# Kernel tuning notes

Measured on AMD Instinct MI355X. Metric: run time of the kernel, lower is better.

The kernel has to match this reference:

```python
import jax, jax.numpy as jnp
import numpy as np

B, C, H, W = 8, 256, 128, 128
P = 7          # patch_size (odd)
N = 500        # n_infer (eval mode)
HIDDEN = C // 16  # reduction=16


def setup_inputs() -> dict:
    key = jax.random.key(0)
    ks = jax.random.split(key, 8)
    def s(k, shape, fan_in):
        return jax.random.normal(k, shape, jnp.float32) * (1.0 / np.sqrt(fan_in))
    return {
        "x_main": jax.random.normal(ks[0], (B, C, H, W), jnp.float32),
        "x_aux": jax.random.normal(ks[1], (B, C, H, W), jnp.float32),
        "scorer_w": s(ks[2], (C,), C),            # 1x1 conv C->1
        "scorer_b": s(ks[3], (1,), C),
        "fc1_w": s(ks[4], (3 * C, HIDDEN), 3 * C),
        "fc1_b": jnp.zeros((HIDDEN,), jnp.float32),
        "fc2_w": s(ks[5], (HIDDEN, C), HIDDEN),
        "fc2_b": jnp.zeros((C,), jnp.float32),
        "proj_w": s(ks[6], (C, C), C),
        "proj_b": jnp.zeros((C,), jnp.float32),
        "n": N,
    }


def _sample_patch_feats(feat, px, py):
    # feat: [C,H,W]; px,py: [n,p,p] pixel coords (align_corners=False convention).
    # Bilinear sample with zero padding, then pool 0.5*(mean+max) over the patch.
    c, h, w = feat.shape
    x0 = jnp.floor(px); y0 = jnp.floor(py)
    wx1 = px - x0; wy1 = py - y0
    def gather(yi, xi):
        valid = ((yi >= 0) & (yi < h) & (xi >= 0) & (xi < w)).astype(feat.dtype)
        yc = jnp.clip(yi, 0, h - 1).astype(jnp.int32)
        xc = jnp.clip(xi, 0, w - 1).astype(jnp.int32)
        return feat[:, yc, xc] * valid  # [C,n,p,p]
    patch = (gather(y0, x0) * ((1 - wy1) * (1 - wx1))
             + gather(y0, x0 + 1) * ((1 - wy1) * wx1)
             + gather(y0 + 1, x0) * (wy1 * (1 - wx1))
             + gather(y0 + 1, x0 + 1) * (wy1 * wx1))  # [C,n,p,p]
    v = 0.5 * (patch.mean(axis=(2, 3)) + patch.max(axis=(2, 3)))  # [C,n]
    return v.T  # [n,C]


def reference(x_main, x_aux, scorer_w, scorer_b, fc1_w, fc1_b, fc2_w, fc2_b, proj_w, proj_b, n):
    b, c, h, w = x_main.shape
    # saliency scores -> topk indices over flattened HW
    score = jax.nn.sigmoid(jnp.einsum('bchw,c->bhw', x_main, scorer_w) + scorer_b[0])
    score = score.reshape(b, h * w)
    _, idx = jax.lax.top_k(score, n)  # [b,n] int32
    idx_y = idx // w
    idx_x = idx - idx_y * w
    # build the (clamped) normalized grid exactly as the torch module does,
    # then convert to pixel coords: px = ((g+1)*W - 1)/2 (align_corners=False)
    r = P // 2
    d = jnp.arange(-r, r + 1, dtype=jnp.float32)
    yy, xx = jnp.meshgrid(d, d, indexing='ij')
    off_x = xx * (2.0 / w); off_y = yy * (2.0 / h)           # [p,p]
    cx = (idx_x.astype(jnp.float32) + 0.5) * (2.0 / w) - 1.0  # [b,n]
    cy = (idx_y.astype(jnp.float32) + 0.5) * (2.0 / h) - 1.0
    gx = jnp.clip(cx[:, :, None, None] + off_x, -1.0, 1.0)    # [b,n,p,p]
    gy = jnp.clip(cy[:, :, None, None] + off_y, -1.0, 1.0)
    px = ((gx + 1.0) * w - 1.0) * 0.5
    py = ((gy + 1.0) * h - 1.0) * 0.5
    sample = jax.vmap(_sample_patch_feats)
    v_main = sample(x_main, px, py)  # [b,n,C]
    v_aux = sample(x_aux, px, py)    # aux_in_proj is Identity (c_main==c_aux)
    # instance-level cross attention
    sim = jnp.einsum('bnc,bmc->bnm', v_main, v_aux) / jnp.sqrt(jnp.float32(c))
    attn = jax.nn.softmax(sim, axis=-1)
    v_hat = jnp.einsum('bnm,bmc->bnc', attn, v_aux)
    # gated fusion MLP
    z = jnp.concatenate([v_main, v_hat, v_main - v_hat], axis=-1)  # [b,n,3C]
    gate = jax.nn.sigmoid(jax.nn.relu(z @ fc1_w + fc1_b) @ fc2_w + fc2_b)
    v_fused = v_main + gate * (v_main - v_hat)
    v_inj = v_fused @ proj_w + proj_b  # [b,n,C]
    # scatter-add reinjection at the topk locations
    inject = jnp.zeros((b, h * w, c), x_main.dtype)
    inject = inject.at[jnp.arange(b)[:, None], idx].add(v_inj)
    inject = inject.reshape(b, h, w, c).transpose(0, 3, 1, 2)
    return x_main + inject
```

## Files before the change

kernel.cpp:

```cpp
#include <hip/hip_runtime.h>
#include <cstdint>
#include <cstddef>

#define HW    16384
#define CCH   256
#define WID   128
#define NB    8
#define NSEL  500
#define NPAD  512
#define CPG   16

__device__ __forceinline__ unsigned key_of(float f) {
  unsigned u = __float_as_uint(f);
  return (u & 0x80000000u) ? ~u : (u | 0x80000000u);
}

__global__ __launch_bounds__(256) void score_copy_kernel(const float* __restrict__ x,
                                                         const float* __restrict__ w,
                                                         float* __restrict__ logits,
                                                         float* __restrict__ out) {
  __shared__ float ws[CCH];
  int tid = threadIdx.x;
  ws[tid] = w[tid];
  __syncthreads();
  int pix = blockIdx.x * 256 + tid;
  int b = pix >> 14, p = pix & (HW - 1);
  const float* xp = x + ((size_t)b << 22) + p;
  float* op = out + ((size_t)b << 22) + p;
  float acc = 0.f;
#pragma unroll 32
  for (int c = 0; c < CCH; c++) {
    float v = xp[(size_t)c * HW];
    acc += v * ws[c];
    __builtin_nontemporal_store(v, &op[(size_t)c * HW]);
  }
  logits[pix] = acc;
}

__global__ __launch_bounds__(1024) void topk_kernel(const float* __restrict__ logits,
                                                    int* __restrict__ idx_out) {
  int b = blockIdx.x, tid = threadIdx.x;
  int lane = tid & 63, wave = tid >> 6;
  const float* lg = logits + (size_t)b * HW;
  __shared__ unsigned histp[16 * 256];
  __shared__ unsigned wtot[4];
  __shared__ unsigned wsum[16];
  __shared__ unsigned bc_prefix;
  __shared__ int bc_want;
  __shared__ int cnt;

  unsigned kreg[16];
#pragma unroll
  for (int j = 0; j < 4; j++) {
    float4 v = *(const float4*)&lg[tid * 16 + j * 4];
    kreg[4 * j + 0] = key_of(v.x);
    kreg[4 * j + 1] = key_of(v.y);
    kreg[4 * j + 2] = key_of(v.z);
    kreg[4 * j + 3] = key_of(v.w);
  }

  unsigned prefix = 0;
  int want = NSEL;
  for (int shift = 24; shift >= 0; shift -= 8) {
#pragma unroll
    for (int q = 0; q < 4; q++) histp[tid + q * 1024] = 0;
    __syncthreads();
    unsigned* myhist = histp + wave * 256;
#pragma unroll
    for (int j = 0; j < 16; j++) {
      unsigned u = kreg[j];
      bool m = (shift == 24) || ((u >> (shift + 8)) == (prefix >> (shift + 8)));
      if (m) atomicAdd(&myhist[(u >> shift) & 255u], 1u);
    }
    __syncthreads();
    unsigned h = 0;
    if (tid < 256) {
#pragma unroll
      for (int w2 = 0; w2 < 16; w2++) h += histp[w2 * 256 + tid];
    }
    unsigned v = h;
#pragma unroll
    for (int o = 1; o < 64; o <<= 1) {
      unsigned t = __shfl_down(v, o);
      if (lane < 64 - o) v += t;
    }
    if (tid < 256 && lane == 0) wtot[wave] = v;
    __syncthreads();
    if (tid < 256) {
      unsigned sfx = v;
      for (int w2 = wave + 1; w2 < 4; w2++) sfx += wtot[w2];
      unsigned above = sfx - h;
      if ((int)sfx >= want && (int)above < want) {
        bc_prefix = prefix | ((unsigned)tid << shift);
        bc_want = want - (int)above;
      }
    }
    __syncthreads();
    prefix = bc_prefix;
    want = bc_want;
  }
  unsigned thr = prefix;

  int local = 0;
#pragma unroll
  for (int j = 0; j < 16; j++) local += (kreg[j] == thr) ? 1 : 0;
  unsigned pv = (unsigned)local;
#pragma unroll
  for (int o = 1; o < 64; o <<= 1) {
    unsigned t = __shfl_up(pv, o);
    if (lane >= o) pv += t;
  }
  if (lane == 63) wsum[wave] = pv;
  if (tid == 0) cnt = 0;
  __syncthreads();
  unsigned woff = 0;
  for (int w2 = 0; w2 < wave; w2++) woff += wsum[w2];
  int rank = (int)(woff + pv) - local;
#pragma unroll
  for (int j = 0; j < 16; j++) {
    unsigned u = kreg[j];
    bool take = (u > thr);
    if (u == thr) { if (rank < want) take = true; rank++; }
    if (take) {
      int s = atomicAdd(&cnt, 1);
      idx_out[b * NPAD + s] = tid * 16 + j;
    }
  }
}

__device__ __forceinline__ void patch_weights(int p, int* xc, int* yc, float* wx, float* wy) {
  int iy = p >> 7, ix = p & (WID - 1);
#pragma unroll
  for (int d = 0; d < 7; d++) {
    int t = ix + d - 3;
    bool in = (t >= 0) && (t < WID);
    xc[d] = in ? t : (t < 0 ? 0 : WID - 1);
    wx[d] = in ? 1.f : 0.5f;
    t = iy + d - 3;
    in = (t >= 0) && (t < WID);
    yc[d] = in ? t : (t < 0 ? 0 : WID - 1);
    wy[d] = in ? 1.f : 0.5f;
  }
}

__global__ __launch_bounds__(512) void gather_dma_kernel(const float* __restrict__ xm,
                                                         const float* __restrict__ xa,
                                                         const int* __restrict__ idx,
                                                         float* __restrict__ vmainT,
                                                         float* __restrict__ vauxT) {
  extern __shared__ float plane2[];
  int g = blockIdx.x, b = blockIdx.y, z = blockIdx.z;
  int tid = threadIdx.x;
  int c0 = g * CPG;
  const float* src = (z == 0 ? xm : xa) + ((size_t)(b * CCH + c0)) * HW;
  float* dst = (z == 0 ? vmainT : vauxT) + (((size_t)(b * CCH + c0)) << 9);

  int t500 = (tid < NSEL) ? tid : 0;
  int p = idx[b * NPAD + t500];
  float wx[7], wy[7];
  int xc[7], yc[7], rb[7];
  patch_weights(p, xc, yc, wx, wy);
#pragma unroll
  for (int d = 0; d < 7; d++) rb[d] = yc[d] * WID;

#pragma unroll
  for (int j = 0; j < 8; j++) {
    int off = (tid + j * 512) * 4;
    __builtin_amdgcn_global_load_lds(
        (const __attribute__((address_space(1))) float*)(src + off),
        (__attribute__((address_space(3))) float*)(plane2 + off), 16, 0, 0);
  }
  __syncthreads();

  for (int c = 0; c < CPG; c++) {
    float* cur = plane2 + ((c & 1) ? HW : 0);
    float* nxt = plane2 + ((c & 1) ? 0 : HW);
    if (c + 1 < CPG) {
      const float* s2 = src + (size_t)(c + 1) * HW;
#pragma unroll
      for (int j = 0; j < 8; j++) {
        int off = (tid + j * 512) * 4;
        __builtin_amdgcn_global_load_lds(
            (const __attribute__((address_space(1))) float*)(s2 + off),
            (__attribute__((address_space(3))) float*)(nxt + off), 16, 0, 0);
      }
    }
    if (tid < NSEL) {
      float s = 0.f, mx = -INFINITY;
#pragma unroll
      for (int dy = 0; dy < 7; dy++) {
        float rs = 0.f, rm = -INFINITY;
        int rbb = rb[dy];
        float wyd = wy[dy];
#pragma unroll
        for (int dx = 0; dx < 7; dx++) {
          float v = cur[rbb + xc[dx]] * wx[dx];
          rs += v;
          rm = fmaxf(rm, v);
        }
        s += rs * wyd;
        mx = fmaxf(mx, rm * wyd);
      }
      dst[((size_t)c << 9) + tid] = 0.5f * (s * (1.f / 49.f) + mx);
    } else {
      dst[((size_t)c << 9) + tid] = 0.f;
    }
    __syncthreads();
  }
}

template <int M, int N, int K, bool AT, bool BT, bool BSHARED, int EPI>
__global__ __launch_bounds__(256) void gemm_kernel(const float* __restrict__ A,
                                                   const float* __restrict__ B,
                                                   float* __restrict__ C,
                                                   const float* __restrict__ bias) {
  constexpr int BM = 64, BN = 64, BK = 16;
  __shared__ float As[BK][BM + 4];
  __shared__ float Bs[BK][BN + 4];
  int tid = threadIdx.x;
  int bx = blockIdx.x, by = blockIdx.y, b = blockIdx.z;
  const float* Ab = A + (size_t)b * M * K;
  const float* Bb = BSHARED ? B : (B + (size_t)b * ((size_t)K * N));
  int tx = tid & 15, ty = tid >> 4;
  float acc[4][4] = {};
  int ar = tid >> 2, ac4 = (tid & 3) * 4;
  int kr = tid >> 4, mc = (tid & 15) * 4;
  int br = tid >> 4, bc4 = (tid & 15) * 4;
  int nr = tid >> 2, kc4 = (tid & 3) * 4;

  auto loadA = [&](int k0) -> float4 {
    if (!AT) return *(const float4*)&Ab[(size_t)(by * BM + ar) * K + k0 + ac4];
    else     return *(const float4*)&Ab[(size_t)(k0 + kr) * M + by * BM + mc];
  };
  auto loadB = [&](int k0) -> float4 {
    if (!BT) return *(const float4*)&Bb[(size_t)(k0 + br) * N + bx * BN + bc4];
    else     return *(const float4*)&Bb[(size_t)(bx * BN + nr) * K + k0 + kc4];
  };

  float4 avr = loadA(0), bvr = loadB(0);
  for (int k0 = 0; k0 < K; k0 += BK) {
    if (!AT) {
      As[ac4 + 0][ar] = avr.x; As[ac4 + 1][ar] = avr.y;
      As[ac4 + 2][ar] = avr.z; As[ac4 + 3][ar] = avr.w;
    } else {
      *(float4*)&As[kr][mc] = avr;
    }
    if (!BT) {
      *(float4*)&Bs[br][bc4] = bvr;
    } else {
      Bs[kc4 + 0][nr] = bvr.x; Bs[kc4 + 1][nr] = bvr.y;
      Bs[kc4 + 2][nr] = bvr.z; Bs[kc4 + 3][nr] = bvr.w;
    }
    __syncthreads();
    if (k0 + BK < K) { avr = loadA(k0 + BK); bvr = loadB(k0 + BK); }
#pragma unroll
    for (int kk = 0; kk < BK; kk++) {
      const float4 a = *(const float4*)&As[kk][ty * 4];
      const float4 bb = *(const float4*)&Bs[kk][tx * 4];
      float av[4] = {a.x, a.y, a.z, a.w};
      float bv[4] = {bb.x, bb.y, bb.z, bb.w};
#pragma unroll
      for (int rr = 0; rr < 4; rr++)
#pragma unroll
        for (int ss = 0; ss < 4; ss++) acc[rr][ss] += av[rr] * bv[ss];
    }
    __syncthreads();
  }
  if (EPI == 2) {
#pragma unroll
    for (int s = 0; s < 4; s++) {
      int col = bx * BN + tx * 4 + s;
      float bv = bias[col];
#pragma unroll
      for (int r = 0; r < 4; r++) {
        int row = by * BM + ty * 4 + r;
        C[((size_t)b * N + col) * M + row] = acc[r][s] + bv;
      }
    }
  } else {
    float scale = (EPI == 1) ? 0.0625f : 1.f;
#pragma unroll
    for (int r = 0; r < 4; r++) {
      int row = by * BM + ty * 4 + r;
#pragma unroll
      for (int s = 0; s < 4; s++) {
        int col = bx * BN + tx * 4 + s;
        C[((size_t)b * M + row) * N + col] = acc[r][s] * scale;
      }
    }
  }
}

__global__ __launch_bounds__(256) void softmax_kernel(float* __restrict__ sim) {
  int i = blockIdx.x, b = blockIdx.y, tid = threadIdx.x;
  float* row = sim + ((size_t)b * NPAD + i) * NPAD;
  float v0 = (tid < NSEL) ? row[tid] : -INFINITY;
  int j1 = tid + 256;
  float v1 = (j1 < NSEL) ? row[j1] : -INFINITY;
  float m = fmaxf(v0, v1);
  for (int o = 32; o; o >>= 1) m = fmaxf(m, __shfl_down(m, o));
  __shared__ float red[4];
  __shared__ float bm, bs;
  int wave = tid >> 6, lane = tid & 63;
  if (lane == 0) red[wave] = m;
  __syncthreads();
  if (tid == 0) bm = fmaxf(fmaxf(red[0], red[1]), fmaxf(red[2], red[3]));
  __syncthreads();
  m = bm;
  float e0 = (tid < NSEL) ? expf(v0 - m) : 0.f;
  float e1 = (j1 < NSEL) ? expf(v1 - m) : 0.f;
  float s = e0 + e1;
  for (int o = 32; o; o >>= 1) s += __shfl_down(s, o);
  if (lane == 0) red[wave] = s;
  __syncthreads();
  if (tid == 0) bs = 1.f / (red[0] + red[1] + red[2] + red[3]);
  __syncthreads();
  row[tid] = e0 * bs;
  row[j1] = e1 * bs;
}

__global__ __launch_bounds__(256) void mlp_kernel(const float* __restrict__ vmainT,
                                                  const float* __restrict__ vhat,
                                                  const float* __restrict__ fc1w,
                                                  const float* __restrict__ fc1b,
                                                  const float* __restrict__ fc2w,
                                                  const float* __restrict__ fc2b,
                                                  float* __restrict__ vfused) {
  int i = blockIdx.x, b = blockIdx.y, c = threadIdx.x;
  size_t base = ((size_t)b * NPAD + i) * CCH + c;
  float vm = vmainT[(((size_t)(b * CCH + c)) << 9) + i];
  float vh = vhat[base], vd = vm - vh;
  const float* w0 = fc1w + (size_t)c * 16;
  const float* w1 = fc1w + (size_t)(256 + c) * 16;
  const float* w2 = fc1w + (size_t)(512 + c) * 16;
  __shared__ float ph[256][17];
  __shared__ float part2[16][17];
  __shared__ float hsh[16];
#pragma unroll
  for (int k = 0; k < 16; k++) ph[c][k] = vm * w0[k] + vh * w1[k] + vd * w2[k];
  __syncthreads();
  int kk = c & 15, g = c >> 4;
  float part = 0.f;
#pragma unroll
  for (int j = 0; j < 16; j++) part += ph[g * 16 + j][kk];
  part2[g][kk] = part;
  __syncthreads();
  if (c < 16) {
    float s = fc1b[c];
#pragma unroll
    for (int g2 = 0; g2 < 16; g2++) s += part2[g2][c];
    hsh[c] = fmaxf(s, 0.f);
  }
  __syncthreads();
  float gte = fc2b[c];
#pragma unroll
  for (int k = 0; k < 16; k++) gte += hsh[k] * fc2w[k * 256 + c];
  gte = 1.f / (1.f + expf(-gte));
  vfused[base] = vm + gte * vd;
}

__global__ __launch_bounds__(256) void scatter_kernel(const int* __restrict__ idx,
                                                      const float* __restrict__ vinjT,
                                                      float* __restrict__ out) {
  int c = blockIdx.x, b = blockIdx.y, t = threadIdx.x;
  float* op = out + ((size_t)(b * CCH + c) << 14);
  const float* vp = vinjT + ((size_t)(b * CCH + c) << 9);
  const int* ib = idx + b * NPAD;
  op[ib[t]] += vp[t];
  int s = t + 256;
  if (s < NSEL) op[ib[s]] += vp[s];
}

extern "C" void kernel_launch(void* const* d_in, const int* in_sizes, int n_in,
                              void* d_out, int out_size, void* d_ws, size_t ws_size,
                              hipStream_t stream) {
  const float* x_main   = (const float*)d_in[0];
  const float* x_aux    = (const float*)d_in[1];
  const float* scorer_w = (const float*)d_in[2];
  const float* fc1_w = (const float*)d_in[4];
  const float* fc1_b = (const float*)d_in[5];
  const float* fc2_w = (const float*)d_in[6];
  const float* fc2_b = (const float*)d_in[7];
  const float* proj_w = (const float*)d_in[8];
  const float* proj_b = (const float*)d_in[9];
  (void)in_sizes; (void)n_in; (void)out_size; (void)ws_size;

  float* ws = (float*)d_ws;
  float* logits = ws;
  int*   idx    = (int*)(ws + 131072);
  float* vmainT = ws + 266240;
  float* vauxT  = ws + 1314816;
  float* vhat   = ws + 2363392;
  float* vfused = ws + 3411968;
  float* sim    = ws + 4460544;
  float* vinjT  = vhat;
  float* out = (float*)d_out;

  score_copy_kernel<<<512, 256, 0, stream>>>(x_main, scorer_w, logits, out);
  topk_kernel<<<NB, 1024, 0, stream>>>(logits, idx);
  gather_dma_kernel<<<dim3(CCH / CPG, NB, 2), 512, 2 * HW * sizeof(float), stream>>>(
      x_main, x_aux, idx, vmainT, vauxT);
  gemm_kernel<NPAD, NPAD, CCH, true, false, false, 1>
      <<<dim3(8, 8, NB), 256, 0, stream>>>(vmainT, vauxT, sim, nullptr);
  softmax_kernel<<<dim3(NPAD, NB), 256, 0, stream>>>(sim);
  gemm_kernel<NPAD, CCH, NPAD, false, true, false, 0>
      <<<dim3(4, 8, NB), 256, 0, stream>>>(sim, vauxT, vhat, nullptr);
  mlp_kernel<<<dim3(NPAD, NB), 256, 0, stream>>>(vmainT, vhat, fc1_w, fc1_b,
                                                 fc2_w, fc2_b, vfused);
  gemm_kernel<NPAD, CCH, CCH, false, false, true, 2>
      <<<dim3(4, 8, NB), 256, 0, stream>>>(vfused, proj_w, vinjT, proj_b);
  scatter_kernel<<<dim3(CCH, NB), 256, 0, stream>>>(idx, vinjT, out);
}
```

Measured before the change: 486.6 us.

## Fuse softmax into attention GEMM and projection into scatter epilogue

The separate softmax kernel is removed. Row max and sum are computed at the start of the attention-times-V GEMM, and exp/normalize is applied while loading the A tile. The projection GEMM now adds its result with bias directly into the output at the top-k pixel locations, which drops the intermediate buffer and the scatter launch. The fused softmax recomputes row statistics once per column block (4x redundant), and the scatter writes are uncoalesced. The score kernel's unroll factor also drops from 32 to 8.

```diff
diff --git a/kernel.cpp b/kernel.cpp
--- a/kernel.cpp
+++ b/kernel.cpp
@@ -28,7 +28,7 @@
   const float* xp = x + ((size_t)b << 22) + p;
   float* op = out + ((size_t)b << 22) + p;
   float acc = 0.f;
-#pragma unroll 32
+#pragma unroll 8
   for (int c = 0; c < CCH; c++) {
     float v = xp[(size_t)c * HW];
     acc += v * ws[c];
@@ -209,50 +209,32 @@
   }
 }
 
-template <int M, int N, int K, bool AT, bool BT, bool BSHARED, int EPI>
-__global__ __launch_bounds__(256) void gemm_kernel(const float* __restrict__ A,
-                                                   const float* __restrict__ B,
-                                                   float* __restrict__ C,
-                                                   const float* __restrict__ bias) {
+template <int M, int N, int K>
+__global__ __launch_bounds__(256) void gemm_tn_kernel(const float* __restrict__ A,
+                                                      const float* __restrict__ B,
+                                                      float* __restrict__ C) {
   constexpr int BM = 64, BN = 64, BK = 16;
   __shared__ float As[BK][BM + 4];
   __shared__ float Bs[BK][BN + 4];
   int tid = threadIdx.x;
   int bx = blockIdx.x, by = blockIdx.y, b = blockIdx.z;
   const float* Ab = A + (size_t)b * M * K;
-  const float* Bb = BSHARED ? B : (B + (size_t)b * ((size_t)K * N));
+  const float* Bb = B + (size_t)b * ((size_t)K * N);
   int tx = tid & 15, ty = tid >> 4;
   float acc[4][4] = {};
-  int ar = tid >> 2, ac4 = (tid & 3) * 4;
   int kr = tid >> 4, mc = (tid & 15) * 4;
   int br = tid >> 4, bc4 = (tid & 15) * 4;
-  int nr = tid >> 2, kc4 = (tid & 3) * 4;
-
-  auto loadA = [&](int k0) -> float4 {
-    if (!AT) return *(const float4*)&Ab[(size_t)(by * BM + ar) * K + k0 + ac4];
-    else     return *(const float4*)&Ab[(size_t)(k0 + kr) * M + by * BM + mc];
-  };
-  auto loadB = [&](int k0) -> float4 {
-    if (!BT) return *(const float4*)&Bb[(size_t)(k0 + br) * N + bx * BN + bc4];
-    else     return *(const float4*)&Bb[(size_t)(bx * BN + nr) * K + k0 + kc4];
-  };
-
-  float4 avr = loadA(0), bvr = loadB(0);
+
+  float4 avr = *(const float4*)&Ab[(size_t)kr * M + by * BM + mc];
+  float4 bvr = *(const float4*)&Bb[(size_t)br * N + bx * BN + bc4];
   for (int k0 = 0; k0 < K; k0 += BK) {
-    if (!AT) {
-      As[ac4 + 0][ar] = avr.x; As[ac4 + 1][ar] = avr.y;
-      As[ac4 + 2][ar] = avr.z; As[ac4 + 3][ar] = avr.w;
-    } else {
-      *(float4*)&As[kr][mc] = avr;
-    }
-    if (!BT) {
-      *(float4*)&Bs[br][bc4] = bvr;
-    } else {
-      Bs[kc4 + 0][nr] = bvr.x; Bs[kc4 + 1][nr] = bvr.y;
-      Bs[kc4 + 2][nr] = bvr.z; Bs[kc4 + 3][nr] = bvr.w;
-    }
-    __syncthreads();
-    if (k0 + BK < K) { avr = loadA(k0 + BK); bvr = loadB(k0 + BK); }
+    *(float4*)&As[kr][mc] = avr;
+    *(float4*)&Bs[br][bc4] = bvr;
+    __syncthreads();
+    if (k0 + BK < K) {
+      avr = *(const float4*)&Ab[(size_t)(k0 + BK + kr) * M + by * BM + mc];
+      bvr = *(const float4*)&Bb[(size_t)(k0 + BK + br) * N + bx * BN + bc4];
+    }
 #pragma unroll
     for (int kk = 0; kk < BK; kk++) {
       const float4 a = *(const float4*)&As[kk][ty * 4];
@@ -266,57 +248,98 @@
     }
     __syncthreads();
   }
-  if (EPI == 2) {
+#pragma unroll
+  for (int r = 0; r < 4; r++) {
+    int row = by * BM + ty * 4 + r;
 #pragma unroll
     for (int s = 0; s < 4; s++) {
       int col = bx * BN + tx * 4 + s;
-      float bv = bias[col];
-#pragma unroll
-      for (int r = 0; r < 4; r++) {
-        int row = by * BM + ty * 4 + r;
-        C[((size_t)b * N + col) * M + row] = acc[r][s] + bv;
-      }
-    }
-  } else {
-    float scale = (EPI == 1) ? 0.0625f : 1.f;
-#pragma unroll
-    for (int r = 0; r < 4; r++) {
-      int row = by * BM + ty * 4 + r;
-#pragma unroll
-      for (int s = 0; s < 4; s++) {
-        int col = bx * BN + tx * 4 + s;
-        C[((size_t)b * M + row) * N + col] = acc[r][s] * scale;
-      }
-    }
-  }
-}
-
-__global__ __launch_bounds__(256) void softmax_kernel(float* __restrict__ sim) {
-  int i = blockIdx.x, b = blockIdx.y, tid = threadIdx.x;
-  float* row = sim + ((size_t)b * NPAD + i) * NPAD;
-  float v0 = (tid < NSEL) ? row[tid] : -INFINITY;
-  int j1 = tid + 256;
-  float v1 = (j1 < NSEL) ? row[j1] : -INFINITY;
-  float m = fmaxf(v0, v1);
-  for (int o = 32; o; o >>= 1) m = fmaxf(m, __shfl_down(m, o));
-  __shared__ float red[4];
-  __shared__ float bm, bs;
-  int wave = tid >> 6, lane = tid & 63;
-  if (lane == 0) red[wave] = m;
-  __syncthreads();
-  if (tid == 0) bm = fmaxf(fmaxf(red[0], red[1]), fmaxf(red[2], red[3]));
-  __syncthreads();
-  m = bm;
-  float e0 = (tid < NSEL) ? expf(v0 - m) : 0.f;
-  float e1 = (j1 < NSEL) ? expf(v1 - m) : 0.f;
-  float s = e0 + e1;
-  for (int o = 32; o; o >>= 1) s += __shfl_down(s, o);
-  if (lane == 0) red[wave] = s;
-  __syncthreads();
-  if (tid == 0) bs = 1.f / (red[0] + red[1] + red[2] + red[3]);
-  __syncthreads();
-  row[tid] = e0 * bs;
-  row[j1] = e1 * bs;
+      C[((size_t)b * M + row) * N + col] = acc[r][s] * 0.0625f;
+    }
+  }
+}
+
+__global__ __launch_bounds__(256) void attn_gemm_kernel(const float* __restrict__ sim,
+                                                        const float* __restrict__ vaux,
+                                                        float* __restrict__ vhat) {
+  constexpr int BM = 64, BN = 64, BK = 16;
+  __shared__ float As[BK][BM + 4];
+  __shared__ float Bs[BK][BN + 4];
+  __shared__ float red[BM][4];
+  __shared__ float sm_m[BM], sm_inv[BM];
+  int tid = threadIdx.x;
+  int bx = blockIdx.x, by = blockIdx.y, b = blockIdx.z;
+  const float* Ab = sim + ((size_t)b * NPAD + by * BM) * NPAD;
+  const float* Bb = vaux + (size_t)b * CCH * NPAD;
+
+  int rr = tid >> 2, q = tid & 3;
+  int j0 = q * 128, j1 = (j0 + 128 < NSEL) ? j0 + 128 : NSEL;
+  const float* rowp = Ab + (size_t)rr * NPAD;
+  float m = -INFINITY;
+  for (int j = j0; j < j1; j += 4) {
+    float4 v = *(const float4*)&rowp[j];
+    m = fmaxf(fmaxf(fmaxf(m, v.x), v.y), fmaxf(v.z, v.w));
+  }
+  red[rr][q] = m;
+  __syncthreads();
+  m = fmaxf(fmaxf(red[rr][0], red[rr][1]), fmaxf(red[rr][2], red[rr][3]));
+  float s = 0.f;
+  for (int j = j0; j < j1; j += 4) {
+    float4 v = *(const float4*)&rowp[j];
+    s += expf(v.x - m) + expf(v.y - m) + expf(v.z - m) + expf(v.w - m);
+  }
+  __syncthreads();
+  red[rr][q] = s;
+  __syncthreads();
+  if (q == 0) {
+    sm_m[rr] = m;
+    sm_inv[rr] = 1.f / (red[rr][0] + red[rr][1] + red[rr][2] + red[rr][3]);
+  }
+  __syncthreads();
+
+  int tx = tid & 15, ty = tid >> 4;
+  float acc[4][4] = {};
+  int ar = tid >> 2, ac4 = (tid & 3) * 4;
+  int nr = tid >> 2, kc4 = (tid & 3) * 4;
+  float mr = sm_m[ar], ir = sm_inv[ar];
+
+  float4 avr = *(const float4*)&Ab[(size_t)ar * NPAD + ac4];
+  float4 bvr = *(const float4*)&Bb[(size_t)(bx * BN + nr) * NPAD + kc4];
+  for (int k0 = 0; k0 < NPAD; k0 += BK) {
+    int kb = k0 + ac4;
+    As[ac4 + 0][ar] = (kb + 0 < NSEL) ? expf(avr.x - mr) * ir : 0.f;
+    As[ac4 + 1][ar] = (kb + 1 < NSEL) ? expf(avr.y - mr) * ir : 0.f;
+    As[ac4 + 2][ar] = (kb + 2 < NSEL) ? expf(avr.z - mr) * ir : 0.f;
+    As[ac4 + 3][ar] = (kb + 3 < NSEL) ? expf(avr.w - mr) * ir : 0.f;
+    Bs[kc4 + 0][nr] = bvr.x; Bs[kc4 + 1][nr] = bvr.y;
+    Bs[kc4 + 2][nr] = bvr.z; Bs[kc4 + 3][nr] = bvr.w;
+    __syncthreads();
+    if (k0 + BK < NPAD) {
+      avr = *(const float4*)&Ab[(size_t)ar * NPAD + k0 + BK + ac4];
+      bvr = *(const float4*)&Bb[(size_t)(bx * BN + nr) * NPAD + k0 + BK + kc4];
+    }
+#pragma unroll
+    for (int kk = 0; kk < BK; kk++) {
+      const float4 a = *(const float4*)&As[kk][ty * 4];
+      const float4 bb = *(const float4*)&Bs[kk][tx * 4];
+      float av[4] = {a.x, a.y, a.z, a.w};
+      float bv[4] = {bb.x, bb.y, bb.z, bb.w};
+#pragma unroll
+      for (int r2 = 0; r2 < 4; r2++)
+#pragma unroll
+        for (int s2 = 0; s2 < 4; s2++) acc[r2][s2] += av[r2] * bv[s2];
+    }
+    __syncthreads();
+  }
+#pragma unroll
+  for (int r = 0; r < 4; r++) {
+    int row = by * BM + ty * 4 + r;
+#pragma unroll
+    for (int s2 = 0; s2 < 4; s2++) {
+      int col = bx * BN + tx * 4 + s2;
+      vhat[((size_t)b * NPAD + row) * CCH + col] = acc[r][s2];
+    }
+  }
 }
 
 __global__ __launch_bounds__(256) void mlp_kernel(const float* __restrict__ vmainT,
@@ -359,16 +382,63 @@
   vfused[base] = vm + gte * vd;
 }
 
-__global__ __launch_bounds__(256) void scatter_kernel(const int* __restrict__ idx,
-                                                      const float* __restrict__ vinjT,
-                                                      float* __restrict__ out) {
-  int c = blockIdx.x, b = blockIdx.y, t = threadIdx.x;
-  float* op = out + ((size_t)(b * CCH + c) << 14);
-  const float* vp = vinjT + ((size_t)(b * CCH + c) << 9);
-  const int* ib = idx + b * NPAD;
-  op[ib[t]] += vp[t];
-  int s = t + 256;
-  if (s < NSEL) op[ib[s]] += vp[s];
+__global__ __launch_bounds__(256) void proj_scatter_kernel(const float* __restrict__ vfused,
+                                                           const float* __restrict__ Bw,
+                                                           const float* __restrict__ bias,
+                                                           const int* __restrict__ idx,
+                                                           float* __restrict__ out) {
+  constexpr int BM = 64, BN = 64, BK = 16;
+  __shared__ float As[BK][BM + 4];
+  __shared__ float Bs[BK][BN + 4];
+  __shared__ int pix[BM];
+  int tid = threadIdx.x;
+  int bx = blockIdx.x, by = blockIdx.y, b = blockIdx.z;
+  if (tid < BM) {
+    int row = by * BM + tid;
+    pix[tid] = (row < NSEL) ? idx[b * NPAD + row] : -1;
+  }
+  const float* Ab = vfused + (size_t)b * NPAD * CCH;
+  int tx = tid & 15, ty = tid >> 4;
+  float acc[4][4] = {};
+  int ar = tid >> 2, ac4 = (tid & 3) * 4;
+  int br = tid >> 4, bc4 = (tid & 15) * 4;
+
+  float4 avr = *(const float4*)&Ab[(size_t)(by * BM + ar) * CCH + ac4];
+  float4 bvr = *(const float4*)&Bw[(size_t)br * CCH + bx * BN + bc4];
+  for (int k0 = 0; k0 < CCH; k0 += BK) {
+    As[ac4 + 0][ar] = avr.x; As[ac4 + 1][ar] = avr.y;
+    As[ac4 + 2][ar] = avr.z; As[ac4 + 3][ar] = avr.w;
+    *(float4*)&Bs[br][bc4] = bvr;
+    __syncthreads();
+    if (k0 + BK < CCH) {
+      avr = *(const float4*)&Ab[(size_t)(by * BM + ar) * CCH + k0 + BK + ac4];
+      bvr = *(const float4*)&Bw[(size_t)(k0 + BK + br) * CCH + bx * BN + bc4];
+    }
+#pragma unroll
+    for (int kk = 0; kk < BK; kk++) {
+      const float4 a = *(const float4*)&As[kk][ty * 4];
+      const float4 bb = *(const float4*)&Bs[kk][tx * 4];
+      float av[4] = {a.x, a.y, a.z, a.w};
+      float bv[4] = {bb.x, bb.y, bb.z, bb.w};
+#pragma unroll
+      for (int rr = 0; rr < 4; rr++)
+#pragma unroll
+        for (int ss = 0; ss < 4; ss++) acc[rr][ss] += av[rr] * bv[ss];
+    }
+    __syncthreads();
+  }
+#pragma unroll
+  for (int r = 0; r < 4; r++) {
+    int p = pix[ty * 4 + r];
+    if (p >= 0) {
+#pragma unroll
+      for (int s = 0; s < 4; s++) {
+        int col = bx * BN + tx * 4 + s;
+        float* o = out + (((size_t)(b * CCH + col)) << 14) + p;
+        *o += acc[r][s] + bias[col];
+      }
+    }
+  }
 }
 
 extern "C" void kernel_launch(void* const* d_in, const int* in_sizes, int n_in,
@@ -393,21 +463,17 @@
   float* vhat   = ws + 2363392;
   float* vfused = ws + 3411968;
   float* sim    = ws + 4460544;
-  float* vinjT  = vhat;
   float* out = (float*)d_out;
 
   score_copy_kernel<<<512, 256, 0, stream>>>(x_main, scorer_w, logits, out);
   topk_kernel<<<NB, 1024, 0, stream>>>(logits, idx);
   gather_dma_kernel<<<dim3(CCH / CPG, NB, 2), 512, 2 * HW * sizeof(float), stream>>>(
       x_main, x_aux, idx, vmainT, vauxT);
-  gemm_kernel<NPAD, NPAD, CCH, true, false, false, 1>
-      <<<dim3(8, 8, NB), 256, 0, stream>>>(vmainT, vauxT, sim, nullptr);
-  softmax_kernel<<<dim3(NPAD, NB), 256, 0, stream>>>(sim);
-  gemm_kernel<NPAD, CCH, NPAD, false, true, false, 0>
-      <<<dim3(4, 8, NB), 256, 0, stream>>>(sim, vauxT, vhat, nullptr);
+  gemm_tn_kernel<NPAD, NPAD, CCH>
+      <<<dim3(8, 8, NB), 256, 0, stream>>>(vmainT, vauxT, sim);
+  attn_gemm_kernel<<<dim3(4, 8, NB), 256, 0, stream>>>(sim, vauxT, vhat);
   mlp_kernel<<<dim3(NPAD, NB), 256, 0, stream>>>(vmainT, vhat, fc1_w, fc1_b,
                                                  fc2_w, fc2_b, vfused);
-  gemm_kernel<NPAD, CCH, CCH, false, false, true, 2>
-      <<<dim3(4, 8, NB), 256, 0, stream>>>(vfused, proj_w, vinjT, proj_b);
-  scatter_kernel<<<dim3(CCH, NB), 256, 0, stream>>>(idx, vinjT, out);
-}
+  proj_scatter_kernel<<<dim3(4, 8, NB), 256, 0, stream>>>(vfused, proj_w, proj_b,
+                                                          idx, out);
+}
```

Result: no change. 495.9 us (+1.9%).
